# Kernel optimization log

Measured on AMD Instinct MI355X. Metric: run time of the kernel, lower is better.

The kernel has to match this reference:

```python
import jax, jax.numpy as jnp
import numpy as np

H = 1024

def setup_inputs() -> dict:
    key = jax.random.key(0)
    ks = jax.random.split(key, 10)
    B, T = 64, 256
    s = 1.0 / np.sqrt(H)  # torch LSTM init scale (uniform(-1/sqrt(H), 1/sqrt(H)))
    return {
        "x": jax.random.normal(ks[0], (B, T, H), jnp.float32),
        "h0": jax.random.normal(ks[1], (1, B, H), jnp.float32),
        "c0": jax.random.normal(ks[2], (1, B, H), jnp.float32),
        "dones": jax.random.randint(ks[3], (B, T), 0, 2).astype(bool),
        "W_ih": jax.random.uniform(ks[4], (4 * H, H), jnp.float32, -s, s),
        "W_hh": jax.random.uniform(ks[5], (4 * H, H), jnp.float32, -s, s),
        "b_ih": jax.random.uniform(ks[6], (4 * H,), jnp.float32, -s, s),
        "b_hh": jax.random.uniform(ks[7], (4 * H,), jnp.float32, -s, s),
    }


def reference(x, h0, c0, dones, W_ih, W_hh, b_ih, b_hh):
    # x: [B,T,H]; h0,c0: [1,B,H]; dones: [B,T] bool
    B, T, _ = x.shape
    xs = jnp.transpose(x, (1, 0, 2))          # [T,B,H]
    ds = jnp.transpose(dones, (1, 0))         # [T,B]
    # Precompute input projections for all steps in one big GEMM
    x_proj = jnp.einsum('tbh,gh->tbg', xs, W_ih) + b_ih + b_hh  # [T,B,4H]

    def step(carry, inp):
        h, c = carry                          # [B,H] each
        xp, done_t = inp                      # [B,4H], [B]
        gates = xp + h @ W_hh.T               # [B,4H]
        i, f, g, o = jnp.split(gates, 4, axis=-1)
        i = jax.nn.sigmoid(i)
        f = jax.nn.sigmoid(f)
        g = jnp.tanh(g)
        o = jax.nn.sigmoid(o)
        c_new = f * c + i * g
        h_new = o * jnp.tanh(c_new)
        # done-based reset applies AFTER emitting the step output
        mask = (~done_t)[:, None].astype(h_new.dtype)
        return (h_new * mask, c_new * mask), h_new

    (h_f, c_f), ys = jax.lax.scan(step, (h0[0], c0[0]), (x_proj, ds))
    out = jnp.tanh(jnp.transpose(ys, (1, 0, 2)))  # activation, [B,T,H]
    return out, h_f[None], c_f[None]
```

## Files before the change

### kernel.cpp

```cpp
#include <hip/hip_runtime.h>

typedef __attribute__((ext_vector_type(8))) short short8;
typedef __attribute__((ext_vector_type(4))) float f32x4;
typedef unsigned long long ull;

__device__ __forceinline__ unsigned short f2bf(float f){
  union { float f; unsigned u; } v; v.f = f;
  return (unsigned short)((v.u + 0x7FFFu + ((v.u >> 16) & 1u)) >> 16);
}
__device__ __forceinline__ float bf2f(unsigned short u){
  union { unsigned u; float f; } v; v.u = ((unsigned)u) << 16; return v.f;
}
__device__ __forceinline__ float fsig(float x){ return 1.f / (1.f + __expf(-x)); }
__device__ __forceinline__ float ftanh(float x){ return 1.f - 2.f / (__expf(2.f * x) + 1.f); }

__device__ __forceinline__ void gld16(const void* g, void* l){
  __builtin_amdgcn_global_load_lds((const __attribute__((address_space(1))) void*)g,
                                   (__attribute__((address_space(3))) void*)l, 16, 0, 0);
}

__global__ __launch_bounds__(256) void cast_x_kernel(const float* __restrict__ x,
                                                     unsigned short* __restrict__ xT){
  const int row = blockIdx.x;
  const int b = row >> 8, t = row & 255;
  float4 v = ((const float4*)(x + (size_t)row * 1024))[threadIdx.x];
  ushort4 o; o.x = f2bf(v.x); o.y = f2bf(v.y); o.z = f2bf(v.z); o.w = f2bf(v.w);
  ((ushort4*)(xT + (size_t)(t * 64 + b) * 1024))[threadIdx.x] = o;
}

__global__ __launch_bounds__(256) void cast_rows_kernel(const float* __restrict__ s,
                                                        unsigned short* __restrict__ d){
  const size_t i = (size_t)blockIdx.x * 256 + threadIdx.x;
  float4 v = ((const float4*)s)[i];
  ushort4 o; o.x = f2bf(v.x); o.y = f2bf(v.y); o.z = f2bf(v.z); o.w = f2bf(v.w);
  ((ushort4*)d)[i] = o;
}

__global__ __launch_bounds__(256) void gemm_xproj_kernel(
    const unsigned short* __restrict__ A,
    const unsigned short* __restrict__ W,
    const float* __restrict__ bih,
    const float* __restrict__ bhh,
    unsigned short* __restrict__ C){
  __shared__ __align__(16) unsigned short As[2][4096];
  __shared__ __align__(16) unsigned short Bs[2][4096];
  const int tid  = threadIdx.x;
  const int lane = tid & 63;
  const int wv   = tid >> 6;
  const int wr   = wv >> 1, wc = wv & 1;
  const int mBase = blockIdx.y << 7;
  const int nBase = blockIdx.x << 7;
  const int lg4 = lane >> 4, lg15 = lane & 15;

  f32x4 acc[4][4] = {};

  auto stage = [&](int buf, int kk){
    #pragma unroll
    for (int rnd = 0; rnd < 2; ++rnd){
      const int s    = tid + (rnd << 8);
      const int row  = s >> 2;
      const int q    = s & 3;
      const int slog = q ^ (row & 3);
      const size_t col = (size_t)(kk << 5) + (slog << 3);
      unsigned short* dA = &As[buf][(size_t)((wv << 6) + (rnd << 8)) << 3];
      unsigned short* dB = &Bs[buf][(size_t)((wv << 6) + (rnd << 8)) << 3];
      gld16(A + (size_t)(mBase + row) * 1024 + col, dA);
      gld16(W + (size_t)(nBase + row) * 1024 + col, dB);
    }
  };

  stage(0, 0);
  __syncthreads();

  for (int kk = 0; kk < 32; ++kk){
    const int buf = kk & 1;
    if (kk != 31) stage(buf ^ 1, kk + 1);
    short8 af[4], bfr[4];
    #pragma unroll
    for (int mi = 0; mi < 4; ++mi){
      const int row = (wr << 6) + (mi << 4) + lg15;
      const int q   = lg4 ^ (row & 3);
      af[mi] = *(const short8*)&As[buf][(row << 5) + (q << 3)];
    }
    #pragma unroll
    for (int ni = 0; ni < 4; ++ni){
      const int row = (wc << 6) + (ni << 4) + lg15;
      const int q   = lg4 ^ (row & 3);
      bfr[ni] = *(const short8*)&Bs[buf][(row << 5) + (q << 3)];
    }
    #pragma unroll
    for (int mi = 0; mi < 4; ++mi)
      #pragma unroll
      for (int ni = 0; ni < 4; ++ni)
        acc[mi][ni] = __builtin_amdgcn_mfma_f32_16x16x32_bf16(af[mi], bfr[ni], acc[mi][ni], 0, 0, 0);
    __syncthreads();
  }

  #pragma unroll
  for (int ni = 0; ni < 4; ++ni){
    const int gcol = nBase + (wc << 6) + (ni << 4) + lg15;
    const float bsum = bih[gcol] + bhh[gcol];
    const int g = gcol >> 10, kk = gcol & 1023;
    const int ktt = kk >> 4, kc = kk & 15;
    #pragma unroll
    for (int mi = 0; mi < 4; ++mi){
      const int grow0 = mBase + (wr << 6) + (mi << 4) + (lg4 << 2);
      const int t = grow0 >> 6, b = grow0 & 63;
      const int btt = b >> 4, rb0 = b & 15;
      const size_t base = ((size_t)((t * 4 + btt) * 64 + ktt) << 10)
                          + (g << 8) + (rb0 << 4) + kc;
      #pragma unroll
      for (int r = 0; r < 4; ++r)
        C[base + (r << 4)] = f2bf(acc[mi][ni][r] + bsum);
    }
  }
}

__device__ __forceinline__ void groupBarrier(unsigned* cnt, unsigned target){
  __syncthreads();
  if (threadIdx.x == 0){
    asm volatile("s_waitcnt vmcnt(0)" ::: "memory");
    __hip_atomic_fetch_add(cnt, 1u, __ATOMIC_RELAXED, __HIP_MEMORY_SCOPE_AGENT);
    while (__hip_atomic_load(cnt, __ATOMIC_RELAXED, __HIP_MEMORY_SCOPE_AGENT) < target)
      __builtin_amdgcn_s_sleep(1);
  }
  __syncthreads();
}

__global__ __launch_bounds__(64) void lstm_steps_kernel(
    const float* __restrict__ Whh,
    const unsigned short* __restrict__ xproj,
    const float* __restrict__ h0,
    const float* __restrict__ c0,
    const int* __restrict__ dones,
    unsigned short* __restrict__ hbuf,
    float* __restrict__ out,
    unsigned* __restrict__ bar){
  __shared__ __align__(16) unsigned short Ws[64 * 1024];
  const int lane = threadIdx.x;
  const int bt = blockIdx.x >> 6;
  const int kt = blockIdx.x & 63;
  const int b0 = bt << 4, k0 = kt << 4;
  const int l15 = lane & 15;
  const int l4  = lane >> 4;

  {
    const int wrow = lane;
    const int g = lane >> 4, j = lane & 15;
    const float* src = Whh + ((size_t)(g << 10) + k0 + j) * 1024;
    for (int c = 0; c < 1024; c += 8){
      float4 v0 = *(const float4*)(src + c);
      float4 v1 = *(const float4*)(src + c + 4);
      short8 pk;
      pk[0] = (short)f2bf(v0.x); pk[1] = (short)f2bf(v0.y);
      pk[2] = (short)f2bf(v0.z); pk[3] = (short)f2bf(v0.w);
      pk[4] = (short)f2bf(v1.x); pk[5] = (short)f2bf(v1.y);
      pk[6] = (short)f2bf(v1.z); pk[7] = (short)f2bf(v1.w);
      const int q = (c >> 3) ^ (wrow & 7);
      *(short8*)&Ws[(wrow << 10) + (q << 3)] = pk;
    }
  }

  ull pk0, pk1, pk2, pk3;
  {
    const int* dp = dones + (size_t)(b0 + l15) * 256 + (l4 << 6);
    ull w = 0;
    for (int j = 0; j < 64; ++j) w |= ((ull)(dp[j] != 0)) << j;
    pk0 = __shfl(w, l15);
    pk1 = __shfl(w, 16 + l15);
    pk2 = __shfl(w, 32 + l15);
    pk3 = __shfl(w, 48 + l15);
  }

  float creg[4];
  {
    float4 cv = *(const float4*)(c0 + (size_t)(b0 + l15) * 1024 + k0 + (l4 << 2));
    creg[0] = cv.x; creg[1] = cv.y; creg[2] = cv.z; creg[3] = cv.w;
  }

  {
    const int i = (kt << 6) + lane;
    const int row = i >> 8;
    const int c4 = (i & 255) << 2;
    float4 v = *(const float4*)(h0 + (size_t)(b0 + row) * 1024 + c4);
    union { ull q; unsigned short s[4]; } p;
    p.s[0] = f2bf(v.x); p.s[1] = f2bf(v.y); p.s[2] = f2bf(v.z); p.s[3] = f2bf(v.w);
    __hip_atomic_store((ull*)hbuf + (size_t)(b0 + row) * 256 + (c4 >> 2), p.q,
                       __ATOMIC_RELAXED, __HIP_MEMORY_SCOPE_AGENT);
  }

  unsigned* cnt = bar + (bt << 5);
  groupBarrier(cnt, 64u);

  const ull* xpb = (const ull*)xproj;
  ull xpc[4];
  {
    const size_t ch0 = ((size_t)(bt * 64 + kt)) << 8;
    #pragma unroll
    for (int g = 0; g < 4; ++g) xpc[g] = xpb[ch0 + (g << 6) + (l15 << 2) + l4];
  }

  union AV { ull q[2]; short8 v; };

  #pragma unroll
  for (int qq = 0; qq < 4; ++qq){
    const ull pkq = (qq == 0) ? pk0 : (qq == 1) ? pk1 : (qq == 2) ? pk2 : pk3;
    for (int t2 = 0; t2 < 64; ++t2){
      const int t = (qq << 6) + t2;
      const ull* hc = (const ull*)hbuf + ((size_t)(t & 1) << 14);
      ull* hn = (ull*)hbuf + ((size_t)((t + 1) & 1) << 14);

      f32x4 acc[4];
      #pragma unroll
      for (int g = 0; g < 4; ++g){
        union { ull q; unsigned short s[4]; } u; u.q = xpc[g];
        #pragma unroll
        for (int r = 0; r < 4; ++r) acc[g][r] = bf2f(u.s[r]);
      }

      const int tn = (t < 255) ? t + 1 : 255;
      ull xpn[4];
      {
        const size_t chn = ((size_t)((tn * 4 + bt) * 64 + kt)) << 8;
        #pragma unroll
        for (int g = 0; g < 4; ++g) xpn[g] = xpb[chn + (g << 6) + (l15 << 2) + l4];
      }

      const ull* hrow = hc + (size_t)(b0 + l15) * 256 + (l4 << 1);
      AV ha[8], hbv[8];
      auto load8 = [&](AV (&hv)[8], int kb){
        #pragma unroll
        for (int j = 0; j < 8; ++j){
          const int ks = (kb << 3) + j;
          hv[j].q[0] = __hip_atomic_load(hrow + (ks << 3),     __ATOMIC_RELAXED, __HIP_MEMORY_SCOPE_AGENT);
          hv[j].q[1] = __hip_atomic_load(hrow + (ks << 3) + 1, __ATOMIC_RELAXED, __HIP_MEMORY_SCOPE_AGENT);
        }
      };
      auto consume = [&](AV (&hv)[8], int kb){
        #pragma unroll
        for (int j = 0; j < 8; ++j){
          const int ks = (kb << 3) + j;
          #pragma unroll
          for (int g = 0; g < 4; ++g){
            const int wrow = (g << 4) + l15;
            const int qs = ((ks << 2) + l4) ^ (wrow & 7);
            const short8 wf = *(const short8*)&Ws[(wrow << 10) + (qs << 3)];
            acc[g] = __builtin_amdgcn_mfma_f32_16x16x32_bf16(wf, hv[j].v, acc[g], 0, 0, 0);
          }
        }
      };
      load8(ha, 0); load8(hbv, 1);
      consume(ha, 0); load8(ha, 2);
      consume(hbv, 1); load8(hbv, 3);
      consume(ha, 2); consume(hbv, 3);

      const float m = ((pkq >> t2) & 1ull) ? 0.f : 1.f;
      float ot4[4], hm4[4];
      unsigned short hb16[4];
      #pragma unroll
      for (int r = 0; r < 4; ++r){
        const float ig = fsig(acc[0][r]);
        const float fg = fsig(acc[1][r]);
        const float gg = ftanh(acc[2][r]);
        const float og = fsig(acc[3][r]);
        const float cn = fg * creg[r] + ig * gg;
        const float hv = og * ftanh(cn);
        ot4[r] = ftanh(hv);
        creg[r] = cn * m;
        const float hm = hv * m;
        hm4[r] = hm;
        hb16[r] = f2bf(hm);
      }

      *(float4*)(out + (size_t)(b0 + l15) * 262144 + ((size_t)t << 10) + k0 + (l4 << 2))
          = make_float4(ot4[0], ot4[1], ot4[2], ot4[3]);
      {
        union { ull q; unsigned short s[4]; } p;
        p.s[0] = hb16[0]; p.s[1] = hb16[1]; p.s[2] = hb16[2]; p.s[3] = hb16[3];
        __hip_atomic_store(hn + (size_t)(b0 + l15) * 256 + (k0 >> 2) + l4, p.q,
                           __ATOMIC_RELAXED, __HIP_MEMORY_SCOPE_AGENT);
      }
      if (qq == 3 && t2 == 63){
        float* hf = out + 16777216 + (size_t)(b0 + l15) * 1024 + k0 + (l4 << 2);
        float* cf = out + 16842752 + (size_t)(b0 + l15) * 1024 + k0 + (l4 << 2);
        *(float4*)hf = make_float4(hm4[0], hm4[1], hm4[2], hm4[3]);
        *(float4*)cf = make_float4(creg[0], creg[1], creg[2], creg[3]);
      }

      groupBarrier(cnt, (unsigned)(t + 2) * 64u);
      #pragma unroll
      for (int g = 0; g < 4; ++g) xpc[g] = xpn[g];
    }
  }
}

extern "C" void kernel_launch(void* const* d_in, const int* in_sizes, int n_in,
                              void* d_out, int out_size, void* d_ws, size_t ws_size,
                              hipStream_t stream){
  const float* x    = (const float*)d_in[0];
  const float* h0   = (const float*)d_in[1];
  const float* c0   = (const float*)d_in[2];
  const int*   dn   = (const int*)d_in[3];
  const float* Wih  = (const float*)d_in[4];
  const float* Whh  = (const float*)d_in[5];
  const float* bih  = (const float*)d_in[6];
  const float* bhh  = (const float*)d_in[7];
  float* out = (float*)d_out;
  char* ws = (char*)d_ws;

  unsigned short* xT    = (unsigned short*)(ws);
  unsigned short* Wib   = (unsigned short*)(ws + 33554432);
  unsigned short* xproj = (unsigned short*)(ws + 41943040);
  unsigned short* hbuf  = (unsigned short*)(ws + 176160768);
  unsigned*       bar   = (unsigned*)(ws + 176422912);

  cast_x_kernel<<<16384, 256, 0, stream>>>(x, xT);
  cast_rows_kernel<<<4096, 256, 0, stream>>>(Wih, Wib);
  gemm_xproj_kernel<<<dim3(32, 128), 256, 0, stream>>>(xT, Wib, bih, bhh, xproj);
  hipMemsetAsync(bar, 0, 1024, stream);

  const float* Whh_ = Whh; const unsigned short* xp_ = xproj;
  const float* h0_ = h0; const float* c0_ = c0; const int* dn_ = dn;
  unsigned short* hb_ = hbuf; float* out_ = out; unsigned* bar_ = bar;
  void* args[] = {&Whh_, &xp_, &h0_, &c0_, &dn_, &hb_, &out_, &bar_};
  hipError_t ce = hipLaunchCooperativeKernel((void*)lstm_steps_kernel, dim3(256), dim3(64),
                                             args, 0, stream);
  if (ce != hipSuccess){
    lstm_steps_kernel<<<256, 64, 0, stream>>>(Whh_, xp_, h0_, c0_, dn_, hb_, out_, bar_);
  }
}
```

Measured before the change: 1.445 ms.

## Replace atomic counter group barrier with per-block step flags polled by lanes

The shared atomic-counter barrier per batch group is replaced with one flag per block that records the latest completed step. Each of the 64 lanes polls one peer block's flag, and the wave proceeds once all flags reach the target. This removes the contended fetch-add and the trailing syncthreads, so a block waits only for h data to be ready rather than for a full round trip. Accumulator initialization from the input projection is also moved after the h loads are issued. Memory ordering still relies on relaxed atomics plus vmcnt waits. Also, hbuf is double-buffered while the new flags only order readers after writers, not writers after readers; a fast block could overwrite a buffer slot that a slower peer is still reading.

```diff
diff --git a/kernel.cpp b/kernel.cpp
--- a/kernel.cpp
+++ b/kernel.cpp
@@ -116,17 +116,6 @@
   }
 }
 
-__device__ __forceinline__ void groupBarrier(unsigned* cnt, unsigned target){
-  __syncthreads();
-  if (threadIdx.x == 0){
-    asm volatile("s_waitcnt vmcnt(0)" ::: "memory");
-    __hip_atomic_fetch_add(cnt, 1u, __ATOMIC_RELAXED, __HIP_MEMORY_SCOPE_AGENT);
-    while (__hip_atomic_load(cnt, __ATOMIC_RELAXED, __HIP_MEMORY_SCOPE_AGENT) < target)
-      __builtin_amdgcn_s_sleep(1);
-  }
-  __syncthreads();
-}
-
 __global__ __launch_bounds__(64) void lstm_steps_kernel(
     const float* __restrict__ Whh,
     const unsigned short* __restrict__ xproj,
@@ -135,7 +124,7 @@
     const int* __restrict__ dones,
     unsigned short* __restrict__ hbuf,
     float* __restrict__ out,
-    unsigned* __restrict__ bar){
+    unsigned* __restrict__ flags){
   __shared__ __align__(16) unsigned short Ws[64 * 1024];
   const int lane = threadIdx.x;
   const int bt = blockIdx.x >> 6;
@@ -188,9 +177,10 @@
     __hip_atomic_store((ull*)hbuf + (size_t)(b0 + row) * 256 + (c4 >> 2), p.q,
                        __ATOMIC_RELAXED, __HIP_MEMORY_SCOPE_AGENT);
   }
-
-  unsigned* cnt = bar + (bt << 5);
-  groupBarrier(cnt, 64u);
+  asm volatile("s_waitcnt vmcnt(0)" ::: "memory");
+  if (lane == 0)
+    __hip_atomic_store(&flags[(bt << 6) + kt], 1u, __ATOMIC_RELAXED, __HIP_MEMORY_SCOPE_AGENT);
+  __syncthreads();
 
   const ull* xpb = (const ull*)xproj;
   ull xpc[4];
@@ -201,6 +191,8 @@
   }
 
   union AV { ull q[2]; short8 v; };
+  const unsigned* myflag = flags + (bt << 6) + lane;
+  unsigned* wflag = flags + (bt << 6) + kt;
 
   #pragma unroll
   for (int qq = 0; qq < 4; ++qq){
@@ -210,20 +202,21 @@
       const ull* hc = (const ull*)hbuf + ((size_t)(t & 1) << 14);
       ull* hn = (ull*)hbuf + ((size_t)((t + 1) & 1) << 14);
 
-      f32x4 acc[4];
-      #pragma unroll
-      for (int g = 0; g < 4; ++g){
-        union { ull q; unsigned short s[4]; } u; u.q = xpc[g];
-        #pragma unroll
-        for (int r = 0; r < 4; ++r) acc[g][r] = bf2f(u.s[r]);
-      }
-
       const int tn = (t < 255) ? t + 1 : 255;
       ull xpn[4];
       {
         const size_t chn = ((size_t)((tn * 4 + bt) * 64 + kt)) << 8;
         #pragma unroll
         for (int g = 0; g < 4; ++g) xpn[g] = xpb[chn + (g << 6) + (l15 << 2) + l4];
+      }
+
+      {
+        const unsigned tgt = (unsigned)t + 1u;
+        unsigned f = __hip_atomic_load(myflag, __ATOMIC_RELAXED, __HIP_MEMORY_SCOPE_AGENT);
+        while (!__all((int)(f >= tgt))){
+          __builtin_amdgcn_s_sleep(1);
+          f = __hip_atomic_load(myflag, __ATOMIC_RELAXED, __HIP_MEMORY_SCOPE_AGENT);
+        }
       }
 
       const ull* hrow = hc + (size_t)(b0 + l15) * 256 + (l4 << 1);
@@ -236,6 +229,17 @@
           hv[j].q[1] = __hip_atomic_load(hrow + (ks << 3) + 1, __ATOMIC_RELAXED, __HIP_MEMORY_SCOPE_AGENT);
         }
       };
+
+      f32x4 acc[4];
+      auto accinit = [&](){
+        #pragma unroll
+        for (int g = 0; g < 4; ++g){
+          union { ull q; unsigned short s[4]; } u; u.q = xpc[g];
+          #pragma unroll
+          for (int r = 0; r < 4; ++r) acc[g][r] = bf2f(u.s[r]);
+        }
+      };
+
       auto consume = [&](AV (&hv)[8], int kb){
         #pragma unroll
         for (int j = 0; j < 8; ++j){
@@ -250,6 +254,7 @@
         }
       };
       load8(ha, 0); load8(hbv, 1);
+      accinit();
       consume(ha, 0); load8(ha, 2);
       consume(hbv, 1); load8(hbv, 3);
       consume(ha, 2); consume(hbv, 3);
@@ -287,7 +292,10 @@
         *(float4*)cf = make_float4(creg[0], creg[1], creg[2], creg[3]);
       }
 
-      groupBarrier(cnt, (unsigned)(t + 2) * 64u);
+      asm volatile("s_waitcnt vmcnt(0)" ::: "memory");
+      if (lane == 0)
+        __hip_atomic_store(wflag, (unsigned)t + 2u, __ATOMIC_RELAXED, __HIP_MEMORY_SCOPE_AGENT);
+
       #pragma unroll
       for (int g = 0; g < 4; ++g) xpc[g] = xpn[g];
     }
@@ -312,20 +320,20 @@
   unsigned short* Wib   = (unsigned short*)(ws + 33554432);
   unsigned short* xproj = (unsigned short*)(ws + 41943040);
   unsigned short* hbuf  = (unsigned short*)(ws + 176160768);
-  unsigned*       bar   = (unsigned*)(ws + 176422912);
+  unsigned*       flags = (unsigned*)(ws + 176422912);
 
   cast_x_kernel<<<16384, 256, 0, stream>>>(x, xT);
   cast_rows_kernel<<<4096, 256, 0, stream>>>(Wih, Wib);
   gemm_xproj_kernel<<<dim3(32, 128), 256, 0, stream>>>(xT, Wib, bih, bhh, xproj);
-  hipMemsetAsync(bar, 0, 1024, stream);
+  hipMemsetAsync(flags, 0, 1024, stream);
 
   const float* Whh_ = Whh; const unsigned short* xp_ = xproj;
   const float* h0_ = h0; const float* c0_ = c0; const int* dn_ = dn;
-  unsigned short* hb_ = hbuf; float* out_ = out; unsigned* bar_ = bar;
-  void* args[] = {&Whh_, &xp_, &h0_, &c0_, &dn_, &hb_, &out_, &bar_};
+  unsigned short* hb_ = hbuf; float* out_ = out; unsigned* fl_ = flags;
+  void* args[] = {&Whh_, &xp_, &h0_, &c0_, &dn_, &hb_, &out_, &fl_};
   hipError_t ce = hipLaunchCooperativeKernel((void*)lstm_steps_kernel, dim3(256), dim3(64),
                                              args, 0, stream);
   if (ce != hipSuccess){
-    lstm_steps_kernel<<<256, 64, 0, stream>>>(Whh_, xp_, h0_, c0_, dn_, hb_, out_, bar_);
-  }
-}
+    lstm_steps_kernel<<<256, 64, 0, stream>>>(Whh_, xp_, h0_, c0_, dn_, hb_, out_, fl_);
+  }
+}
```

Result: slower. 1.688 ms (+16.8%).

## Interleave two batch chains per block with split arrive/wait barriers

Applied to the files above, without the earlier changes.

Each block now handles two independent 16-row batch tiles, so it runs on 128 blocks instead of 256, and it alternates a recurrent step between the two chains. The barrier is split into an arrive (an atomic add after the h store) and a later wait (a spin before the next step of the same chain). This lets one chain's synchronisation latency overlap with the other chain's MFMA work, and halves the number of blocks that each load W_hh into LDS. The cost is half as many CUs in use and twice the serial compute per block per step. The output store is also moved after the arrive.

```diff
diff --git a/kernel.cpp b/kernel.cpp
--- a/kernel.cpp
+++ b/kernel.cpp
@@ -116,17 +116,6 @@
   }
 }
 
-__device__ __forceinline__ void groupBarrier(unsigned* cnt, unsigned target){
-  __syncthreads();
-  if (threadIdx.x == 0){
-    asm volatile("s_waitcnt vmcnt(0)" ::: "memory");
-    __hip_atomic_fetch_add(cnt, 1u, __ATOMIC_RELAXED, __HIP_MEMORY_SCOPE_AGENT);
-    while (__hip_atomic_load(cnt, __ATOMIC_RELAXED, __HIP_MEMORY_SCOPE_AGENT) < target)
-      __builtin_amdgcn_s_sleep(1);
-  }
-  __syncthreads();
-}
-
 __global__ __launch_bounds__(64) void lstm_steps_kernel(
     const float* __restrict__ Whh,
     const unsigned short* __restrict__ xproj,
@@ -138,9 +127,11 @@
     unsigned* __restrict__ bar){
   __shared__ __align__(16) unsigned short Ws[64 * 1024];
   const int lane = threadIdx.x;
-  const int bt = blockIdx.x >> 6;
+  const int p  = blockIdx.x >> 6;
   const int kt = blockIdx.x & 63;
-  const int b0 = bt << 4, k0 = kt << 4;
+  const int btA = p * 2, btB = p * 2 + 1;
+  const int b0A = btA << 4, b0B = btB << 4;
+  const int k0 = kt << 4;
   const int l15 = lane & 15;
   const int l4  = lane >> 4;
 
@@ -161,135 +152,176 @@
     }
   }
 
-  ull pk0, pk1, pk2, pk3;
-  {
-    const int* dp = dones + (size_t)(b0 + l15) * 256 + (l4 << 6);
+  ull pkA0, pkA1, pkA2, pkA3, pkB0, pkB1, pkB2, pkB3;
+  {
+    const int* dpA = dones + (size_t)(b0A + l15) * 256 + (l4 << 6);
     ull w = 0;
-    for (int j = 0; j < 64; ++j) w |= ((ull)(dp[j] != 0)) << j;
-    pk0 = __shfl(w, l15);
-    pk1 = __shfl(w, 16 + l15);
-    pk2 = __shfl(w, 32 + l15);
-    pk3 = __shfl(w, 48 + l15);
-  }
-
-  float creg[4];
-  {
-    float4 cv = *(const float4*)(c0 + (size_t)(b0 + l15) * 1024 + k0 + (l4 << 2));
-    creg[0] = cv.x; creg[1] = cv.y; creg[2] = cv.z; creg[3] = cv.w;
-  }
+    for (int j = 0; j < 64; ++j) w |= ((ull)(dpA[j] != 0)) << j;
+    pkA0 = __shfl(w, l15); pkA1 = __shfl(w, 16 + l15);
+    pkA2 = __shfl(w, 32 + l15); pkA3 = __shfl(w, 48 + l15);
+    const int* dpB = dones + (size_t)(b0B + l15) * 256 + (l4 << 6);
+    w = 0;
+    for (int j = 0; j < 64; ++j) w |= ((ull)(dpB[j] != 0)) << j;
+    pkB0 = __shfl(w, l15); pkB1 = __shfl(w, 16 + l15);
+    pkB2 = __shfl(w, 32 + l15); pkB3 = __shfl(w, 48 + l15);
+  }
+
+  float cregA[4], cregB[4];
+  {
+    float4 cv = *(const float4*)(c0 + (size_t)(b0A + l15) * 1024 + k0 + (l4 << 2));
+    cregA[0] = cv.x; cregA[1] = cv.y; cregA[2] = cv.z; cregA[3] = cv.w;
+    cv = *(const float4*)(c0 + (size_t)(b0B + l15) * 1024 + k0 + (l4 << 2));
+    cregB[0] = cv.x; cregB[1] = cv.y; cregB[2] = cv.z; cregB[3] = cv.w;
+  }
+
+  ull* hbA = (ull*)hbuf + (size_t)btA * 8192;
+  ull* hbB = (ull*)hbuf + (size_t)btB * 8192;
 
   {
     const int i = (kt << 6) + lane;
     const int row = i >> 8;
     const int c4 = (i & 255) << 2;
-    float4 v = *(const float4*)(h0 + (size_t)(b0 + row) * 1024 + c4);
-    union { ull q; unsigned short s[4]; } p;
-    p.s[0] = f2bf(v.x); p.s[1] = f2bf(v.y); p.s[2] = f2bf(v.z); p.s[3] = f2bf(v.w);
-    __hip_atomic_store((ull*)hbuf + (size_t)(b0 + row) * 256 + (c4 >> 2), p.q,
+    float4 v = *(const float4*)(h0 + (size_t)(b0A + row) * 1024 + c4);
+    union { ull q; unsigned short s[4]; } pq;
+    pq.s[0] = f2bf(v.x); pq.s[1] = f2bf(v.y); pq.s[2] = f2bf(v.z); pq.s[3] = f2bf(v.w);
+    __hip_atomic_store(hbA + (size_t)row * 256 + (c4 >> 2), pq.q,
                        __ATOMIC_RELAXED, __HIP_MEMORY_SCOPE_AGENT);
-  }
-
-  unsigned* cnt = bar + (bt << 5);
-  groupBarrier(cnt, 64u);
+    v = *(const float4*)(h0 + (size_t)(b0B + row) * 1024 + c4);
+    pq.s[0] = f2bf(v.x); pq.s[1] = f2bf(v.y); pq.s[2] = f2bf(v.z); pq.s[3] = f2bf(v.w);
+    __hip_atomic_store(hbB + (size_t)row * 256 + (c4 >> 2), pq.q,
+                       __ATOMIC_RELAXED, __HIP_MEMORY_SCOPE_AGENT);
+  }
+
+  unsigned* cntA = bar + (btA << 6);
+  unsigned* cntB = bar + (btB << 6);
+  asm volatile("s_waitcnt vmcnt(0)" ::: "memory");
+  if (lane == 0){
+    __hip_atomic_fetch_add(cntA, 1u, __ATOMIC_RELAXED, __HIP_MEMORY_SCOPE_AGENT);
+    __hip_atomic_fetch_add(cntB, 1u, __ATOMIC_RELAXED, __HIP_MEMORY_SCOPE_AGENT);
+  }
+  __syncthreads();
 
   const ull* xpb = (const ull*)xproj;
-  ull xpc[4];
-  {
-    const size_t ch0 = ((size_t)(bt * 64 + kt)) << 8;
-    #pragma unroll
-    for (int g = 0; g < 4; ++g) xpc[g] = xpb[ch0 + (g << 6) + (l15 << 2) + l4];
+  ull xpcA[4], xpcB[4];
+  {
+    const size_t chA = ((size_t)(btA * 64 + kt)) << 8;
+    const size_t chB = ((size_t)(btB * 64 + kt)) << 8;
+    #pragma unroll
+    for (int g = 0; g < 4; ++g){
+      xpcA[g] = xpb[chA + (g << 6) + (l15 << 2) + l4];
+      xpcB[g] = xpb[chB + (g << 6) + (l15 << 2) + l4];
+    }
   }
 
   union AV { ull q[2]; short8 v; };
 
-  #pragma unroll
-  for (int qq = 0; qq < 4; ++qq){
-    const ull pkq = (qq == 0) ? pk0 : (qq == 1) ? pk1 : (qq == 2) ? pk2 : pk3;
-    for (int t2 = 0; t2 < 64; ++t2){
-      const int t = (qq << 6) + t2;
-      const ull* hc = (const ull*)hbuf + ((size_t)(t & 1) << 14);
-      ull* hn = (ull*)hbuf + ((size_t)((t + 1) & 1) << 14);
-
-      f32x4 acc[4];
+  auto chainStep = [&](int t, ull pkq, int t2, int b0, ull* hb, unsigned* cnt,
+                       float (&creg)[4], ull (&xpc)[4]) {
+    const ull* hc = hb + ((size_t)(t & 1) << 12);
+    ull* hn = hb + ((size_t)((t + 1) & 1) << 12);
+
+    {
+      const unsigned tgt = ((unsigned)t + 1u) << 6;
+      while (__hip_atomic_load(cnt, __ATOMIC_RELAXED, __HIP_MEMORY_SCOPE_AGENT) < tgt)
+        __builtin_amdgcn_s_sleep(1);
+    }
+
+    const ull* hrow = hc + (size_t)l15 * 256 + (l4 << 1);
+    AV ha[8], hbv[8];
+    auto load8 = [&](AV (&hv)[8], int kb){
+      #pragma unroll
+      for (int j = 0; j < 8; ++j){
+        const int ks = (kb << 3) + j;
+        hv[j].q[0] = __hip_atomic_load(hrow + (ks << 3),     __ATOMIC_RELAXED, __HIP_MEMORY_SCOPE_AGENT);
+        hv[j].q[1] = __hip_atomic_load(hrow + (ks << 3) + 1, __ATOMIC_RELAXED, __HIP_MEMORY_SCOPE_AGENT);
+      }
+    };
+    f32x4 acc[4];
+    auto accinit = [&](){
       #pragma unroll
       for (int g = 0; g < 4; ++g){
         union { ull q; unsigned short s[4]; } u; u.q = xpc[g];
         #pragma unroll
         for (int r = 0; r < 4; ++r) acc[g][r] = bf2f(u.s[r]);
       }
+    };
+    auto consume = [&](AV (&hv)[8], int kb){
+      #pragma unroll
+      for (int j = 0; j < 8; ++j){
+        const int ks = (kb << 3) + j;
+        #pragma unroll
+        for (int g = 0; g < 4; ++g){
+          const int wrow = (g << 4) + l15;
+          const int qs = ((ks << 2) + l4) ^ (wrow & 7);
+          const short8 wf = *(const short8*)&Ws[(wrow << 10) + (qs << 3)];
+          acc[g] = __builtin_amdgcn_mfma_f32_16x16x32_bf16(wf, hv[j].v, acc[g], 0, 0, 0);
+        }
+      }
+    };
+    load8(ha, 0); load8(hbv, 1);
+    accinit();
+    consume(ha, 0); load8(ha, 2);
+    consume(hbv, 1); load8(hbv, 3);
+    consume(ha, 2); consume(hbv, 3);
+
+    const float m = ((pkq >> t2) & 1ull) ? 0.f : 1.f;
+    float ot4[4], hm4[4];
+    unsigned short hb16[4];
+    #pragma unroll
+    for (int r = 0; r < 4; ++r){
+      const float ig = fsig(acc[0][r]);
+      const float fg = fsig(acc[1][r]);
+      const float gg = ftanh(acc[2][r]);
+      const float og = fsig(acc[3][r]);
+      const float cn = fg * creg[r] + ig * gg;
+      const float hv = og * ftanh(cn);
+      ot4[r] = ftanh(hv);
+      creg[r] = cn * m;
+      const float hm = hv * m;
+      hm4[r] = hm;
+      hb16[r] = f2bf(hm);
+    }
+
+    {
+      union { ull q; unsigned short s[4]; } pq;
+      pq.s[0] = hb16[0]; pq.s[1] = hb16[1]; pq.s[2] = hb16[2]; pq.s[3] = hb16[3];
+      __hip_atomic_store(hn + (size_t)l15 * 256 + (k0 >> 2) + l4, pq.q,
+                         __ATOMIC_RELAXED, __HIP_MEMORY_SCOPE_AGENT);
+    }
+    asm volatile("s_waitcnt vmcnt(0)" ::: "memory");
+    if (lane == 0)
+      __hip_atomic_fetch_add(cnt, 1u, __ATOMIC_RELAXED, __HIP_MEMORY_SCOPE_AGENT);
+
+    *(float4*)(out + (size_t)(b0 + l15) * 262144 + ((size_t)t << 10) + k0 + (l4 << 2))
+        = make_float4(ot4[0], ot4[1], ot4[2], ot4[3]);
+    if (t == 255){
+      float* hf = out + 16777216 + (size_t)(b0 + l15) * 1024 + k0 + (l4 << 2);
+      float* cf = out + 16842752 + (size_t)(b0 + l15) * 1024 + k0 + (l4 << 2);
+      *(float4*)hf = make_float4(hm4[0], hm4[1], hm4[2], hm4[3]);
+      *(float4*)cf = make_float4(creg[0], creg[1], creg[2], creg[3]);
+    }
+  };
+
+  #pragma unroll
+  for (int qq = 0; qq < 4; ++qq){
+    const ull pkqA = (qq == 0) ? pkA0 : (qq == 1) ? pkA1 : (qq == 2) ? pkA2 : pkA3;
+    const ull pkqB = (qq == 0) ? pkB0 : (qq == 1) ? pkB1 : (qq == 2) ? pkB2 : pkB3;
+    for (int t2 = 0; t2 < 64; ++t2){
+      const int t = (qq << 6) + t2;
+
+      chainStep(t, pkqA, t2, b0A, hbA, cntA, cregA, xpcA);
+      chainStep(t, pkqB, t2, b0B, hbB, cntB, cregB, xpcB);
 
       const int tn = (t < 255) ? t + 1 : 255;
-      ull xpn[4];
       {
-        const size_t chn = ((size_t)((tn * 4 + bt) * 64 + kt)) << 8;
+        const size_t chA = ((size_t)((tn * 4 + btA) * 64 + kt)) << 8;
+        const size_t chB = ((size_t)((tn * 4 + btB) * 64 + kt)) << 8;
         #pragma unroll
-        for (int g = 0; g < 4; ++g) xpn[g] = xpb[chn + (g << 6) + (l15 << 2) + l4];
+        for (int g = 0; g < 4; ++g){
+          xpcA[g] = xpb[chA + (g << 6) + (l15 << 2) + l4];
+          xpcB[g] = xpb[chB + (g << 6) + (l15 << 2) + l4];
+        }
       }
-
-      const ull* hrow = hc + (size_t)(b0 + l15) * 256 + (l4 << 1);
-      AV ha[8], hbv[8];
-      auto load8 = [&](AV (&hv)[8], int kb){
-        #pragma unroll
-        for (int j = 0; j < 8; ++j){
-          const int ks = (kb << 3) + j;
-          hv[j].q[0] = __hip_atomic_load(hrow + (ks << 3),     __ATOMIC_RELAXED, __HIP_MEMORY_SCOPE_AGENT);
-          hv[j].q[1] = __hip_atomic_load(hrow + (ks << 3) + 1, __ATOMIC_RELAXED, __HIP_MEMORY_SCOPE_AGENT);
-        }
-      };
-      auto consume = [&](AV (&hv)[8], int kb){
-        #pragma unroll
-        for (int j = 0; j < 8; ++j){
-          const int ks = (kb << 3) + j;
-          #pragma unroll
-          for (int g = 0; g < 4; ++g){
-            const int wrow = (g << 4) + l15;
-            const int qs = ((ks << 2) + l4) ^ (wrow & 7);
-            const short8 wf = *(const short8*)&Ws[(wrow << 10) + (qs << 3)];
-            acc[g] = __builtin_amdgcn_mfma_f32_16x16x32_bf16(wf, hv[j].v, acc[g], 0, 0, 0);
-          }
-        }
-      };
-      load8(ha, 0); load8(hbv, 1);
-      consume(ha, 0); load8(ha, 2);
-      consume(hbv, 1); load8(hbv, 3);
-      consume(ha, 2); consume(hbv, 3);
-
-      const float m = ((pkq >> t2) & 1ull) ? 0.f : 1.f;
-      float ot4[4], hm4[4];
-      unsigned short hb16[4];
-      #pragma unroll
-      for (int r = 0; r < 4; ++r){
-        const float ig = fsig(acc[0][r]);
-        const float fg = fsig(acc[1][r]);
-        const float gg = ftanh(acc[2][r]);
-        const float og = fsig(acc[3][r]);
-        const float cn = fg * creg[r] + ig * gg;
-        const float hv = og * ftanh(cn);
-        ot4[r] = ftanh(hv);
-        creg[r] = cn * m;
-        const float hm = hv * m;
-        hm4[r] = hm;
-        hb16[r] = f2bf(hm);
-      }
-
-      *(float4*)(out + (size_t)(b0 + l15) * 262144 + ((size_t)t << 10) + k0 + (l4 << 2))
-          = make_float4(ot4[0], ot4[1], ot4[2], ot4[3]);
-      {
-        union { ull q; unsigned short s[4]; } p;
-        p.s[0] = hb16[0]; p.s[1] = hb16[1]; p.s[2] = hb16[2]; p.s[3] = hb16[3];
-        __hip_atomic_store(hn + (size_t)(b0 + l15) * 256 + (k0 >> 2) + l4, p.q,
-                           __ATOMIC_RELAXED, __HIP_MEMORY_SCOPE_AGENT);
-      }
-      if (qq == 3 && t2 == 63){
-        float* hf = out + 16777216 + (size_t)(b0 + l15) * 1024 + k0 + (l4 << 2);
-        float* cf = out + 16842752 + (size_t)(b0 + l15) * 1024 + k0 + (l4 << 2);
-        *(float4*)hf = make_float4(hm4[0], hm4[1], hm4[2], hm4[3]);
-        *(float4*)cf = make_float4(creg[0], creg[1], creg[2], creg[3]);
-      }
-
-      groupBarrier(cnt, (unsigned)(t + 2) * 64u);
-      #pragma unroll
-      for (int g = 0; g < 4; ++g) xpc[g] = xpn[g];
     }
   }
 }
@@ -323,9 +355,9 @@
   const float* h0_ = h0; const float* c0_ = c0; const int* dn_ = dn;
   unsigned short* hb_ = hbuf; float* out_ = out; unsigned* bar_ = bar;
   void* args[] = {&Whh_, &xp_, &h0_, &c0_, &dn_, &hb_, &out_, &bar_};
-  hipError_t ce = hipLaunchCooperativeKernel((void*)lstm_steps_kernel, dim3(256), dim3(64),
+  hipError_t ce = hipLaunchCooperativeKernel((void*)lstm_steps_kernel, dim3(128), dim3(64),
                                              args, 0, stream);
   if (ce != hipSuccess){
-    lstm_steps_kernel<<<256, 64, 0, stream>>>(Whh_, xp_, h0_, c0_, dn_, hb_, out_, bar_);
-  }
-}
+    lstm_steps_kernel<<<128, 64, 0, stream>>>(Whh_, xp_, h0_, c0_, dn_, hb_, out_, bar_);
+  }
+}
```

Measured after the change: 2.181 ms. +50.9%, slower.
